# Performance work log

Measured on AMD Instinct MI355X. Metric: run time of the kernel, lower is better.

The kernel has to match this reference:

```python
import jax, jax.numpy as jnp
import numpy as np

TAU = 1.0  # gumbel-softmax temperature (self.tau)


def setup_inputs() -> dict:
    key = jax.random.key(0)
    k1, k2 = jax.random.split(key)
    K = 256
    # x0 is a one-hot categorical image: [B, H, W, K]
    idx = jax.random.randint(k1, (32, 64, 64), 0, K)
    x0 = jax.nn.one_hot(idx, K, dtype=jnp.float32)
    # standard DDPM-style beta schedule values in (1e-4, 0.02)
    beta_values = jax.random.uniform(k2, (1000,), jnp.float32, 1e-4, 0.02)
    return {"x0": x0, "beta_values": beta_values, "t": 500}


def reference(x0, beta_values, t):
    K = x0.shape[-1]
    # Each Q_i = (1-b_i) I + b_i/K * ones. These matrices commute and are
    # closed under multiplication: prod_{i<t} Q_i = abar I + (1-abar) ones/K
    # with abar = prod_{i<t}(1 - b_i). This is the exact closed form of the
    # original O(t) serial matmul loop (row-stochasticity fixes the ones/K
    # coefficient to 1-abar).
    alpha_bar = jnp.prod(1.0 - beta_values[:t])
    bar_Q_t = alpha_bar * jnp.eye(K, dtype=x0.dtype) \
        + (1.0 - alpha_bar) * jnp.ones((K, K), dtype=x0.dtype) / K
    p = jnp.einsum('bhwk,kj->bhwj', x0, bar_Q_t)
    logits = jnp.log(p)
    # gumbel-softmax sample (noise is independent of the float inputs)
    u = jax.random.uniform(jax.random.key(1), logits.shape, logits.dtype,
                           minval=1e-9, maxval=1.0)
    gumbel = -jnp.log(-jnp.log(u))
    return jax.nn.softmax((logits + gumbel) / TAU, axis=-1)
```

## Files before the change

### kernel.cpp

```cpp
#include <hip/hip_runtime.h>
#include <stdint.h>

#define N_PIX     131072u
#define KDIM      256u

__device__ __forceinline__ uint32_t rotl32(uint32_t v, int r) {
  return (v << r) | (v >> (32 - r));
}

__device__ __forceinline__ uint32_t threefry_xor_01(uint32_t c0, uint32_t c1) {
  const uint32_t ks0 = 0u;
  const uint32_t ks1 = 1u;
  const uint32_t ks2 = 0x1BD11BDAu ^ ks0 ^ ks1;
  uint32_t x0 = c0 + ks0;
  uint32_t x1 = c1 + ks1;
#define TF_R(r) { x0 += x1; x1 = rotl32(x1, (r)); x1 ^= x0; }
  TF_R(13) TF_R(15) TF_R(26) TF_R(6)
  x0 += ks1; x1 += ks2 + 1u;
  TF_R(17) TF_R(29) TF_R(16) TF_R(24)
  x0 += ks2; x1 += ks0 + 2u;
  TF_R(13) TF_R(15) TF_R(26) TF_R(6)
  x0 += ks0; x1 += ks1 + 3u;
  TF_R(17) TF_R(29) TF_R(16) TF_R(24)
  x0 += ks1; x1 += ks2 + 4u;
  TF_R(13) TF_R(15) TF_R(26) TF_R(6)
  x0 += ks2; x1 += ks0 + 5u;
#undef TF_R
  return x0 ^ x1;
}

__device__ __forceinline__ float bits_to_uniform(uint32_t bits) {
  float f = __uint_as_float((bits >> 9) | 0x3F800000u) - 1.0f;
  float u = f * 1.0f + 1e-9f;
  return fmaxf(1e-9f, u);
}

__global__ void abar_kernel(const float* __restrict__ beta,
                            const int* __restrict__ t_ptr,
                            float* __restrict__ ws) {
  const int t = t_ptr[0];
  const int lane = threadIdx.x;
  float p = 1.0f;
  for (int i = lane; i < t; i += 64) p *= (1.0f - beta[i]);
  for (int off = 32; off; off >>= 1) p *= __shfl_down(p, off);
  if (lane == 0) ws[0] = p;
}

__global__ __launch_bounds__(128) void
diffusion_sample_kernel(const float2* __restrict__ x0,
                        const float* __restrict__ abar_p,
                        float2* __restrict__ out) {
  const int tid = threadIdx.x;
  const uint32_t P = blockIdx.x;
  const uint32_t j0 = P * KDIM + 2u * (uint32_t)tid;

  const float abar = abar_p[0];
  const float poff = (1.0f - abar) * (1.0f / 256.0f);

  const uint32_t bits0 = threefry_xor_01(0u, j0);
  const uint32_t bits1 = threefry_xor_01(0u, j0 + 1u);

  const float u0 = bits_to_uniform(bits0);
  const float u1 = bits_to_uniform(bits1);
  const float w0 = -1.0f / logf(u0);
  const float w1 = -1.0f / logf(u1);

  const float2 xv = x0[(size_t)P * 128u + (size_t)tid];
  const float n0 = fmaf(xv.x, abar, poff) * w0;
  const float n1 = fmaf(xv.y, abar, poff) * w1;

  float r = n0 + n1;
  for (int off = 32; off; off >>= 1) r += __shfl_down(r, off);
  __shared__ float sh[2];
  if ((tid & 63) == 0) sh[tid >> 6] = r;
  __syncthreads();
  const float sinv = 1.0f / (sh[0] + sh[1]);

  out[(size_t)P * 128u + (size_t)tid] = make_float2(n0 * sinv, n1 * sinv);
}

extern "C" void kernel_launch(void* const* d_in, const int* in_sizes, int n_in,
                              void* d_out, int out_size, void* d_ws, size_t ws_size,
                              hipStream_t stream) {
  const float* x0   = (const float*)d_in[0];
  const float* beta = (const float*)d_in[1];
  const int*   t    = (const int*)d_in[2];
  float* out = (float*)d_out;
  float* ws  = (float*)d_ws;

  abar_kernel<<<1, 64, 0, stream>>>(beta, t, ws);
  diffusion_sample_kernel<<<N_PIX, 128, 0, stream>>>(
      (const float2*)x0, ws, (float2*)out);
}
```

Measured before the change: 90.85 us.

## Map one wavefront per pixel with float4 I/O and fast log/rcp intrinsics

Restructures the sampling kernel so each 64-lane wavefront handles a whole 256-class pixel, with four pixels per 256-thread block. Each lane now loads and stores float4 values. The cross-wave shared-memory reduction and __syncthreads are replaced by an xor-shuffle wave reduction. The precise logf and divisions become __log2f and hardware rcp approximations, and output uses nontemporal stores. This cuts block count, synchronization and transcendental cost, at the risk of small numerical differences from the approximate log and reciprocal.

```diff
diff --git a/kernel.cpp b/kernel.cpp
--- a/kernel.cpp
+++ b/kernel.cpp
@@ -4,15 +4,17 @@
 #define N_PIX     131072u
 #define KDIM      256u
 
+typedef float f32x4 __attribute__((ext_vector_type(4)));
+
 __device__ __forceinline__ uint32_t rotl32(uint32_t v, int r) {
   return (v << r) | (v >> (32 - r));
 }
 
-__device__ __forceinline__ uint32_t threefry_xor_01(uint32_t c0, uint32_t c1) {
+__device__ __forceinline__ uint32_t threefry_xor_01(uint32_t c1) {
   const uint32_t ks0 = 0u;
   const uint32_t ks1 = 1u;
-  const uint32_t ks2 = 0x1BD11BDAu ^ ks0 ^ ks1;
-  uint32_t x0 = c0 + ks0;
+  const uint32_t ks2 = 0x1BD11BDBu;
+  uint32_t x0 = 0u + ks0;
   uint32_t x1 = c1 + ks1;
 #define TF_R(r) { x0 += x1; x1 = rotl32(x1, (r)); x1 ^= x0; }
   TF_R(13) TF_R(15) TF_R(26) TF_R(6)
@@ -29,10 +31,12 @@
   return x0 ^ x1;
 }
 
-__device__ __forceinline__ float bits_to_uniform(uint32_t bits) {
+__device__ __forceinline__ float gumbel_weight(uint32_t bits) {
   float f = __uint_as_float((bits >> 9) | 0x3F800000u) - 1.0f;
-  float u = f * 1.0f + 1e-9f;
-  return fmaxf(1e-9f, u);
+  float u = fmaxf(1e-9f, f + 1e-9f);
+  float L = __log2f(u);
+  L = fminf(L, -1.0e-20f);
+  return -1.44269504088896340736f * __builtin_amdgcn_rcpf(L);
 }
 
 __global__ void abar_kernel(const float* __restrict__ beta,
@@ -46,37 +50,39 @@
   if (lane == 0) ws[0] = p;
 }
 
-__global__ __launch_bounds__(128) void
-diffusion_sample_kernel(const float2* __restrict__ x0,
+__global__ __launch_bounds__(256) void
+diffusion_sample_kernel(const f32x4* __restrict__ x0,
                         const float* __restrict__ abar_p,
-                        float2* __restrict__ out) {
-  const int tid = threadIdx.x;
-  const uint32_t P = blockIdx.x;
-  const uint32_t j0 = P * KDIM + 2u * (uint32_t)tid;
+                        f32x4* __restrict__ out) {
+  const int lane = threadIdx.x & 63;
+  const int wave = threadIdx.x >> 6;
+  const uint32_t P = blockIdx.x * 4u + (uint32_t)wave;
+  const uint32_t j0 = P * KDIM + (uint32_t)lane * 4u;
 
   const float abar = abar_p[0];
   const float poff = (1.0f - abar) * (1.0f / 256.0f);
 
-  const uint32_t bits0 = threefry_xor_01(0u, j0);
-  const uint32_t bits1 = threefry_xor_01(0u, j0 + 1u);
+  const uint32_t b0 = threefry_xor_01(j0);
+  const uint32_t b1 = threefry_xor_01(j0 + 1u);
+  const uint32_t b2 = threefry_xor_01(j0 + 2u);
+  const uint32_t b3 = threefry_xor_01(j0 + 3u);
 
-  const float u0 = bits_to_uniform(bits0);
-  const float u1 = bits_to_uniform(bits1);
-  const float w0 = -1.0f / logf(u0);
-  const float w1 = -1.0f / logf(u1);
+  const size_t v = (size_t)P * 64u + (size_t)lane;
+  const f32x4 xv = x0[v];
 
-  const float2 xv = x0[(size_t)P * 128u + (size_t)tid];
-  const float n0 = fmaf(xv.x, abar, poff) * w0;
-  const float n1 = fmaf(xv.y, abar, poff) * w1;
+  const float n0 = fmaf(xv.x, abar, poff) * gumbel_weight(b0);
+  const float n1 = fmaf(xv.y, abar, poff) * gumbel_weight(b1);
+  const float n2 = fmaf(xv.z, abar, poff) * gumbel_weight(b2);
+  const float n3 = fmaf(xv.w, abar, poff) * gumbel_weight(b3);
 
-  float r = n0 + n1;
-  for (int off = 32; off; off >>= 1) r += __shfl_down(r, off);
-  __shared__ float sh[2];
-  if ((tid & 63) == 0) sh[tid >> 6] = r;
-  __syncthreads();
-  const float sinv = 1.0f / (sh[0] + sh[1]);
+  float r = (n0 + n1) + (n2 + n3);
+  #pragma unroll
+  for (int off = 32; off; off >>= 1) r += __shfl_xor(r, off);
+  const float sinv = __builtin_amdgcn_rcpf(r);
 
-  out[(size_t)P * 128u + (size_t)tid] = make_float2(n0 * sinv, n1 * sinv);
+  f32x4 o;
+  o.x = n0 * sinv; o.y = n1 * sinv; o.z = n2 * sinv; o.w = n3 * sinv;
+  __builtin_nontemporal_store(o, &out[v]);
 }
 
 extern "C" void kernel_launch(void* const* d_in, const int* in_sizes, int n_in,
@@ -89,6 +95,6 @@
   float* ws  = (float*)d_ws;
 
   abar_kernel<<<1, 64, 0, stream>>>(beta, t, ws);
-  diffusion_sample_kernel<<<N_PIX, 128, 0, stream>>>(
-      (const float2*)x0, ws, (float2*)out);
+  diffusion_sample_kernel<<<N_PIX / 4u, 256, 0, stream>>>(
+      (const f32x4*)x0, ws, (f32x4*)out);
 }
```

Result: faster. 78.82 us (-13.2%).
